# Kernel optimization log

Measured on AMD Instinct MI355X. Metric: run time of the kernel, lower is better.

The kernel has to match this reference:

```python
import jax, jax.numpy as jnp
import numpy as np
import math

B, L, D = 2, 2048, 1024
H, DH, R, MAX_ORDER = 16, 64, 512, 5
NUM_BASIS = MAX_ORDER + 1  # min(basis_rank=512, 6)


def setup_inputs() -> dict:
    key = jax.random.key(0)
    ks = jax.random.split(key, 8)
    s = 0.02
    return {
        "hidden_states": jax.random.normal(ks[0], (B, L, D), jnp.float32),
        "attention_mask": jnp.zeros((B, 1, 1, L), jnp.float32),
        "Wq": jax.random.normal(ks[1], (D, D), jnp.float32) * s,
        "bq": jnp.zeros((D,), jnp.float32),
        "Wk": jax.random.normal(ks[2], (D, D), jnp.float32) * s,
        "bk": jnp.zeros((D,), jnp.float32),
        "Wv": jax.random.normal(ks[3], (D, D), jnp.float32) * s,
        "bv": jnp.zeros((D,), jnp.float32),
        "q_proj_weight": jax.random.normal(ks[4], (H, DH, R), jnp.float32) / math.sqrt(DH),
        "k_proj_weight": jax.random.normal(ks[5], (H, DH, R), jnp.float32) / math.sqrt(DH),
        "coefficients": jax.random.normal(ks[6], (H, NUM_BASIS), jnp.float32) * s,
    }


def _basis_bias(coefficients, seq_len, dtype):
    # rel[i, j] = (j - i) / (L - 1), clamped to [-1, 1]; DCT basis cos(pi * k * x)
    pos = jnp.arange(seq_len, dtype=dtype)
    x = jnp.clip((pos[None, :] - pos[:, None]) / max(seq_len - 1, 1), -1.0, 1.0)
    k = jnp.arange(NUM_BASIS, dtype=dtype)
    tk = jnp.cos(jnp.pi * x[..., None] * k)  # [L, L, K]
    return jnp.einsum('hk,ijk->hij', coefficients, tk)  # [H, L, L]


def reference(hidden_states, attention_mask, Wq, bq, Wk, bk, Wv, bv,
              q_proj_weight, k_proj_weight, coefficients):
    b, l, _ = hidden_states.shape

    def shape_heads(x):
        return x.reshape(b, l, H, DH).transpose(0, 2, 1, 3)  # [B, H, L, DH]

    q = shape_heads(hidden_states @ Wq.T + bq)
    k = shape_heads(hidden_states @ Wk.T + bk)
    v = shape_heads(hidden_states @ Wv.T + bv)

    qp = jnp.einsum('bhld,hdr->bhlr', q, q_proj_weight)
    kp = jnp.einsum('bhld,hdr->bhlr', k, k_proj_weight)
    scores = jnp.einsum('bhlr,bhmr->bhlm', qp, kp) / math.sqrt(R)

    bias = _basis_bias(coefficients, l, scores.dtype)
    scores = scores + bias[None] + attention_mask

    probs = jax.nn.softmax(scores, axis=-1)  # dropout is identity in eval
    ctx = jnp.einsum('bhlm,bhmd->bhld', probs, v)
    return ctx.transpose(0, 2, 1, 3).reshape(b, l, H * DH)
```

## Files before the change

### kernel.cpp

```cpp
#include <hip/hip_runtime.h>


typedef unsigned short ushort_t;
typedef unsigned long long ull_t;
typedef __attribute__((ext_vector_type(8))) short bf16x8;
typedef __attribute__((ext_vector_type(4))) float f32x4;

#define LOG2E 1.4426950408889634f
#define PI_F 3.14159265358979323846f

__device__ inline f32x4 mfma16(bf16x8 a, bf16x8 b, f32x4 c) {
  return __builtin_amdgcn_mfma_f32_16x16x32_bf16(a, b, c, 0, 0, 0);
}
__device__ inline void load_lds16(const void* g, void* l) {
  __builtin_amdgcn_global_load_lds((const __attribute__((address_space(1))) unsigned int*)g,
                                   (__attribute__((address_space(3))) unsigned int*)l, 16, 0, 0);
}
__device__ inline ushort_t f2bf(float f) {
  union { float f; unsigned int u; } v; v.f = f;
  unsigned int u = v.u;
  return (ushort_t)((u + 0x7fffu + ((u >> 16) & 1u)) >> 16);
}
__device__ inline unsigned cvt_pk_bf16(float lo, float hi) {
  unsigned r;
  asm("v_cvt_pk_bf16_f32 %0, %1, %2" : "=v"(r) : "v"(lo), "v"(hi));
  return r;
}
#if __has_builtin(__builtin_amdgcn_exp2f)
__device__ inline float exp2_(float x) { return __builtin_amdgcn_exp2f(x); }
#else
__device__ inline float exp2_(float x) { return exp2f(x); }
#endif

__global__ __launch_bounds__(256) void k_prep(
    const float* __restrict__ hidden, const float* __restrict__ Wk,
    const float* __restrict__ Wv, const float* __restrict__ qpw,
    const float* __restrict__ kpw, const float* __restrict__ coef,
    const float* __restrict__ maskp,
    ushort_t* __restrict__ hb, ushort_t* __restrict__ w3, float* __restrict__ Ah,
    ushort_t* __restrict__ ke, ushort_t* __restrict__ qe) {
  __shared__ float tile[64][65];
  const int blk = blockIdx.x, tid = threadIdx.x;
  if (blk < 64) {
    int h = blk >> 2, db = (blk & 3) * 16;
    int dp = tid & 63, d0 = db + (tid >> 6) * 4;
    float acc[4] = {0.f, 0.f, 0.f, 0.f};
    const float* kh = kpw + (size_t)h * 64 * 512;
    const float* qr = qpw + ((size_t)h * 64 + d0) * 512;
    for (int rc = 0; rc < 8; rc++) {
      __syncthreads();
      #pragma unroll
      for (int i = 0; i < 4; i++) {
        int idx = i * 256 + tid;
        int d = idx >> 4, c4 = idx & 15;
        float4 v = *(const float4*)(kh + (size_t)d * 512 + rc * 64 + c4 * 4);
        *(float4*)(&tile[d][c4 * 4]) = v;
      }
      __syncthreads();
      for (int rr = 0; rr < 64; rr += 4) {
        float4 wk = *(const float4*)(&tile[dp][rr]);
        int r = rc * 64 + rr;
        #pragma unroll
        for (int i = 0; i < 4; i++) {
          float4 wq = *(const float4*)(qr + i * 512 + r);
          acc[i] += wq.x * wk.x + wq.y * wk.y + wq.z * wk.z + wq.w * wk.w;
        }
      }
    }
    #pragma unroll
    for (int i = 0; i < 4; i++)
      Ah[((size_t)h * 64 + d0 + i) * 64 + dp] = acc[i] * (0.044194173824159216f * LOG2E);
  } else if (blk < 3136) {
    const float* in;
    ushort_t* out;
    int base = blk - 64;
    if (base < 2048) { in = hidden; out = hb; }
    else if (base < 2560) { in = Wk; out = w3 + 1048576; base -= 2048; }
    else { in = Wv; out = w3 + 2097152; base -= 2560; }
    int i = (base * 256 + tid) * 8;
    float4 v0 = *(const float4*)(in + i);
    float4 v1 = *(const float4*)(in + i + 4);
    ull_t pk0 = (ull_t)f2bf(v0.x) | ((ull_t)f2bf(v0.y) << 16)
              | ((ull_t)f2bf(v0.z) << 32) | ((ull_t)f2bf(v0.w) << 48);
    ull_t pk1 = (ull_t)f2bf(v1.x) | ((ull_t)f2bf(v1.y) << 16)
              | ((ull_t)f2bf(v1.z) << 32) | ((ull_t)f2bf(v1.w) << 48);
    ull_t* dst = (ull_t*)(out + i);
    dst[0] = pk0;
    dst[1] = pk1;
  } else if (blk < 3152) {
    int i = (blk - 3136) * 256 + tid;
    int bb = i >> 11, m = i & 2047;
    float base = PI_F * (float)m * (1.0f / 2047.0f);
    ushort_t row[32];
    row[0] = f2bf(1.0f);
    #pragma unroll
    for (int k = 1; k <= 5; k++) {
      float a = base * (float)k;
      row[2 * k - 1] = f2bf(cosf(a));
      row[2 * k]     = f2bf(sinf(a));
    }
    row[11] = f2bf(maskp[bb * 2048 + m] * LOG2E);
    #pragma unroll
    for (int j = 12; j < 32; j++) row[j] = 0;
    ull_t* dst = (ull_t*)(ke + ((size_t)(bb * 2048 + m)) * 32);
    #pragma unroll
    for (int j = 0; j < 4; j++) {
      ull_t pk = 0;
      #pragma unroll
      for (int e = 0; e < 4; e++) pk |= (ull_t)row[j * 4 + e] << (16 * e);
      dst[j] = pk;
    }
  } else {
    int i = (blk - 3152) * 256 + tid;
    int h = i >> 11, q = i & 2047;
    float base = PI_F * (float)q * (1.0f / 2047.0f);
    ushort_t row[32];
    row[0] = f2bf(coef[h * 6] * LOG2E);
    #pragma unroll
    for (int k = 1; k <= 5; k++) {
      float ck = coef[h * 6 + k] * LOG2E;
      float a = base * (float)k;
      row[2 * k - 1] = f2bf(ck * cosf(a));
      row[2 * k]     = f2bf(ck * sinf(a));
    }
    row[11] = f2bf(1.0f);
    #pragma unroll
    for (int j = 12; j < 32; j++) row[j] = 0;
    ull_t* dst = (ull_t*)(qe + ((size_t)(h * 2048 + q)) * 32);
    #pragma unroll
    for (int j = 0; j < 4; j++) {
      ull_t pk = 0;
      #pragma unroll
      for (int e = 0; e < 4; e++) pk |= (ull_t)row[j * 4 + e] << (16 * e);
      dst[j] = pk;
    }
  }
}

__global__ __launch_bounds__(256) void k_wq(
    const float* __restrict__ Wq, const float* __restrict__ Ah,
    const float* __restrict__ bq, ushort_t* __restrict__ w3, float* __restrict__ bq2) {
  __shared__ float wq_s[64][65];
  __shared__ float ah_s[64][65];
  int h = blockIdx.y, ct = blockIdx.x;
  int t = threadIdx.x;
  #pragma unroll
  for (int i = 0; i < 16; i++) {
    int idx = i * 256 + t, r = idx >> 6, c = idx & 63;
    wq_s[r][c] = Wq[((size_t)h * 64 + r) * 1024 + ct * 64 + c];
    ah_s[r][c] = Ah[((size_t)h * 64 + r) * 64 + c];
  }
  __syncthreads();
  int dp = t >> 2, cg = (t & 3) * 16;
  float acc[16];
  #pragma unroll
  for (int j = 0; j < 16; j++) acc[j] = 0.f;
  for (int d = 0; d < 64; d++) {
    float a = ah_s[d][dp];
    #pragma unroll
    for (int j = 0; j < 16; j++) acc[j] += a * wq_s[d][cg + j];
  }
  ushort_t* orow = w3 + ((size_t)h * 64 + dp) * 1024 + ct * 64 + cg;
  #pragma unroll
  for (int j = 0; j < 16; j += 4) {
    ull_t pk = (ull_t)f2bf(acc[j]) | ((ull_t)f2bf(acc[j + 1]) << 16)
             | ((ull_t)f2bf(acc[j + 2]) << 32) | ((ull_t)f2bf(acc[j + 3]) << 48);
    *(ull_t*)(orow + j) = pk;
  }
  if (ct == 0 && t < 64) {
    float bsum = 0.f;
    for (int d = 0; d < 64; d++) bsum += bq[h * 64 + d] * ah_s[d][t];
    bq2[h * 64 + t] = bsum;
  }
}

__global__ __launch_bounds__(256) void k_gemm(
    const ushort_t* __restrict__ hb, const ushort_t* __restrict__ w3,
    const float* __restrict__ bq2, const float* __restrict__ bk,
    const float* __restrict__ bv, ushort_t* __restrict__ qk, ushort_t* __restrict__ vT) {
  __shared__ ushort_t Asm[128 * 64];
  __shared__ ushort_t Bsm[128 * 64];
  const int tid = threadIdx.x, w = tid >> 6, l = tid & 63, g = l >> 4, l15 = l & 15;
  const int raw = blockIdx.x;
  const int id = (raw & 7) * 96 + (raw >> 3);
  const bool isv = id >= 512;
  int bx, by;
  const ushort_t *Aptr, *Bptr;
  if (!isv) { bx = id & 31; by = id >> 5; Aptr = hb; Bptr = w3; }
  else { int id2 = id - 512; bx = id2 & 7; by = id2 >> 3; Aptr = w3 + 2048 * 1024; Bptr = hb; }
  const int mbase = bx * 128, nbase = by * 128;
  const int wrow = (w >> 1) * 64, wcol = (w & 1) * 64;
  f32x4 zero4 = {0.f, 0.f, 0.f, 0.f};
  f32x4 acc[4][4];
  #pragma unroll
  for (int i = 0; i < 4; i++)
    #pragma unroll
    for (int j = 0; j < 4; j++) acc[i][j] = zero4;

  for (int kt = 0; kt < 16; ++kt) {
    __syncthreads();
    #pragma unroll
    for (int i = 0; i < 4; i++) {
      int r0 = i * 32 + w * 8;
      int r = r0 + (l >> 3);
      int cs = (l & 7) ^ (r & 7);
      load_lds16(Aptr + (size_t)(mbase + r) * 1024 + kt * 64 + cs * 8, &Asm[r0 * 64]);
      load_lds16(Bptr + (size_t)(nbase + r) * 1024 + kt * 64 + cs * 8, &Bsm[r0 * 64]);
    }
    __syncthreads();
    #pragma unroll
    for (int ks = 0; ks < 2; ks++) {
      bf16x8 a[4], bfr[4];
      #pragma unroll
      for (int rt = 0; rt < 4; rt++) {
        int r = wrow + rt * 16 + l15;
        a[rt] = *(const bf16x8*)(&Asm[r * 64 + (((ks * 4 + g) ^ (r & 7)) << 3)]);
      }
      #pragma unroll
      for (int ct = 0; ct < 4; ct++) {
        int r = wcol + ct * 16 + l15;
        bfr[ct] = *(const bf16x8*)(&Bsm[r * 64 + (((ks * 4 + g) ^ (r & 7)) << 3)]);
      }
      #pragma unroll
      for (int rt = 0; rt < 4; rt++)
        #pragma unroll
        for (int ct = 0; ct < 4; ct++)
          acc[rt][ct] = mfma16(a[rt], bfr[ct], acc[rt][ct]);
    }
  }
  if (!isv) {
    #pragma unroll
    for (int ct = 0; ct < 4; ct++) {
      int n = nbase + wcol + ct * 16 + l15;
      float bias = (n < 1024) ? bq2[n] : bk[n - 1024];
      #pragma unroll
      for (int rt = 0; rt < 4; rt++)
        #pragma unroll
        for (int reg = 0; reg < 4; reg++) {
          int m = mbase + wrow + rt * 16 + g * 4 + reg;
          qk[(size_t)m * 2048 + n] = f2bf(acc[rt][ct][reg] + bias);
        }
    }
  } else {
    #pragma unroll
    for (int rt = 0; rt < 4; rt++)
      #pragma unroll
      for (int reg = 0; reg < 4; reg++) {
        int dg = mbase + wrow + rt * 16 + g * 4 + reg;
        float bias = bv[dg];
        ushort_t* vrow = vT + ((size_t)(dg >> 6)) * 131072 + (size_t)(dg & 63) * 2048;
        #pragma unroll
        for (int ct = 0; ct < 4; ct++) {
          int mg = nbase + wcol + ct * 16 + l15;
          vrow[((size_t)(mg >> 11)) * 2097152 + (mg & 2047)] = f2bf(acc[rt][ct][reg] + bias);
        }
      }
  }
}

__global__ __launch_bounds__(512, 4) void k_attn(
    const ushort_t* __restrict__ qk, const ushort_t* __restrict__ vT,
    const ushort_t* __restrict__ qe, const ushort_t* __restrict__ ke,
    float* __restrict__ out) {
  __shared__ ushort_t k_sm[2][64][64];
  __shared__ ushort_t vt_sm[2][64][64];
  __shared__ ushort_t ke_sm[2][64][32];
  const int tid = threadIdx.x, w = tid >> 6, l = tid & 63, g = l >> 4, l15 = l & 15;
  const int e01 = l15 & 3, a0 = (l15 >> 2) & 1;
  const int lr = l >> 3, lc = l & 7;
  const int bid = blockIdx.x, xcd = bid & 7, slot = bid >> 3;
  const int bh = xcd * 4 + (slot & 3), qb = slot >> 2;
  const int b = bh >> 4, h = bh & 15;
  const int wrow = qb * 128 + w * 16;
  const int q = wrow + l15;

  const ushort_t* kbase = qk + 1024 + h * 64;
  const ushort_t* vT_bh = vT + (size_t)bh * 64 * 2048;
  const ushort_t* ke_b = ke + (size_t)b * 2048 * 32;

  auto stage = [&](int t, int bi) {
    int kvb = t * 64;
    {
      int m = w * 8 + lr;
      int sc = lc ^ ((lr & 3) | ((w & 1) << 2));
      load_lds16(kbase + (size_t)(b * 2048 + kvb + m) * 2048 + sc * 8,
                 &k_sm[bi][w * 8][0]);
    }
    {
      int d = w * 8 + lr;
      int sc = lc ^ ((lr & 3) | ((w & 1) << 2));
      load_lds16(vT_bh + (size_t)d * 2048 + kvb + sc * 8,
                 &vt_sm[bi][w * 8][0]);
    }
    if (w < 4) {
      int ml = l >> 2, c = l & 3;
      load_lds16(ke_b + (size_t)(kvb + w * 16 + ml) * 32 + ((c ^ (ml & 3)) << 3),
                 &ke_sm[bi][w * 16][0]);
    }
  };

  stage(0, 0);

  bf16x8 qf[2], qfe;
  {
    const ushort_t* qpr = qk + (size_t)(b * 2048 + q) * 2048 + h * 64 + g * 8;
    qf[0] = *(const bf16x8*)(qpr);
    qf[1] = *(const bf16x8*)(qpr + 32);
    qfe = *(const bf16x8*)(qe + ((size_t)(h * 2048 + q)) * 32 + g * 8);
  }

  f32x4 zero4 = {0.f, 0.f, 0.f, 0.f};
  f32x4 ctx[4];
  float lrow = 0.f;
  #pragma unroll
  for (int dt = 0; dt < 4; dt++) ctx[dt] = zero4;

  __syncthreads();

  for (int t = 0; t < 32; t++) {
    const int bi = t & 1;
    if (t < 31) stage(t + 1, bi ^ 1);

    f32x4 ST[4];
    #pragma unroll
    for (int mt = 0; mt < 4; mt++) ST[mt] = zero4;
    #pragma unroll
    for (int ks = 0; ks < 2; ks++) {
      #pragma unroll
      for (int mt = 0; mt < 4; mt++) {
        int mr = (mt >> 1) * 32 + (l15 >> 2) * 8 + (mt & 1) * 4 + e01;
        int pc = (ks * 4 + g) ^ (e01 | (a0 << 2));
        bf16x8 af = *(const bf16x8*)(&k_sm[bi][mr][pc * 8]);
        ST[mt] = mfma16(af, qf[ks], ST[mt]);
      }
    }
    #pragma unroll
    for (int mt = 0; mt < 4; mt++) {
      int mr = (mt >> 1) * 32 + (l15 >> 2) * 8 + (mt & 1) * 4 + e01;
      bf16x8 af = *(const bf16x8*)(&ke_sm[bi][mr][(g ^ e01) * 8]);
      ST[mt] = mfma16(af, qfe, ST[mt]);
    }

    float pv[4][4];
    #pragma unroll
    for (int mt = 0; mt < 4; mt++) {
      pv[mt][0] = exp2_(ST[mt][0]);
      pv[mt][1] = exp2_(ST[mt][1]);
      pv[mt][2] = exp2_(ST[mt][2]);
      pv[mt][3] = exp2_(ST[mt][3]);
      lrow += pv[mt][0] + pv[mt][1] + pv[mt][2] + pv[mt][3];
    }
    bf16x8 pf[2];
    {
      union { unsigned u[4]; bf16x8 v; } pk0, pk1;
      pk0.u[0] = cvt_pk_bf16(pv[0][0], pv[0][1]);
      pk0.u[1] = cvt_pk_bf16(pv[0][2], pv[0][3]);
      pk0.u[2] = cvt_pk_bf16(pv[1][0], pv[1][1]);
      pk0.u[3] = cvt_pk_bf16(pv[1][2], pv[1][3]);
      pk1.u[0] = cvt_pk_bf16(pv[2][0], pv[2][1]);
      pk1.u[1] = cvt_pk_bf16(pv[2][2], pv[2][3]);
      pk1.u[2] = cvt_pk_bf16(pv[3][0], pv[3][1]);
      pk1.u[3] = cvt_pk_bf16(pv[3][2], pv[3][3]);
      pf[0] = pk0.v;
      pf[1] = pk1.v;
    }

    #pragma unroll
    for (int kp = 0; kp < 2; kp++) {
      #pragma unroll
      for (int dt = 0; dt < 4; dt++) {
        int d = dt * 16 + l15;
        int pc = (kp * 4 + g) ^ (e01 | (((l15 >> 3) & 1) << 2));
        bf16x8 vf = *(const bf16x8*)(&vt_sm[bi][d][pc * 8]);
        ctx[dt] = mfma16(vf, pf[kp], ctx[dt]);
      }
    }

    __syncthreads();
  }

  lrow += __shfl_xor(lrow, 16);
  lrow += __shfl_xor(lrow, 32);
  float inv = 1.0f / lrow;
  float* op = out + ((size_t)(b * 2048 + q)) * 1024 + h * 64 + g * 4;
  #pragma unroll
  for (int dt = 0; dt < 4; dt++) {
    float4 o = {ctx[dt][0] * inv, ctx[dt][1] * inv, ctx[dt][2] * inv, ctx[dt][3] * inv};
    *(float4*)(op + dt * 16) = o;
  }
}

extern "C" void kernel_launch(void* const* d_in, const int* in_sizes, int n_in,
                              void* d_out, int out_size, void* d_ws, size_t ws_size,
                              hipStream_t stream) {
  const float* hidden = (const float*)d_in[0];
  const float* maskp  = (const float*)d_in[1];
  const float* Wq     = (const float*)d_in[2];
  const float* bq     = (const float*)d_in[3];
  const float* Wk     = (const float*)d_in[4];
  const float* bk     = (const float*)d_in[5];
  const float* Wv     = (const float*)d_in[6];
  const float* bv     = (const float*)d_in[7];
  const float* qpw    = (const float*)d_in[8];
  const float* kpw    = (const float*)d_in[9];
  const float* coef   = (const float*)d_in[10];

  char* ws = (char*)d_ws;
  ushort_t* keb   = (ushort_t*)(ws);
  ushort_t* hb    = (ushort_t*)(ws + 262144);
  ushort_t* w3    = (ushort_t*)(ws + 8650752);
  float*    Ah    = (float*)(ws + 14942208);
  float*    bq2   = (float*)(ws + 15204352);
  ushort_t* qeb   = (ushort_t*)(ws + 15208448);
  ushort_t* qkb   = (ushort_t*)(ws + 17305600);
  ushort_t* vTb   = (ushort_t*)(ws + 34082816);

  k_prep<<<3280, 256, 0, stream>>>(hidden, Wk, Wv, qpw, kpw, coef, maskp,
                                   hb, w3, Ah, keb, qeb);
  k_wq<<<dim3(16, 16), 256, 0, stream>>>(Wq, Ah, bq, w3, bq2);
  k_gemm<<<768, 256, 0, stream>>>(hb, w3, bq2, bk, bv, qkb, vTb);
  k_attn<<<512, 512, 0, stream>>>(qkb, vTb, qeb, keb, (float*)d_out);
}
```

Before: 136.0 us.

## Give each attention wave two query sub-tiles to reuse K/V fragments

The attention kernel drops from 8 waves to 4 waves per block, and each wave now handles 32 query rows as two 16-row sub-tiles. Each K, Ke and V fragment read from LDS is reused for two MFMAs, which halves LDS reads per unit of work, and the staging loads are split across fewer waves. The cost is higher register pressure (doubled accumulators and P fragments), fewer waves per CU to hide latency, and a changed launch bound of 256 threads with 2 blocks.

```diff
diff --git a/kernel.cpp b/kernel.cpp
--- a/kernel.cpp
+++ b/kernel.cpp
@@ -258,7 +258,7 @@
   }
 }
 
-__global__ __launch_bounds__(512, 4) void k_attn(
+__global__ __launch_bounds__(256, 2) void k_attn(
     const ushort_t* __restrict__ qk, const ushort_t* __restrict__ vT,
     const ushort_t* __restrict__ qe, const ushort_t* __restrict__ ke,
     float* __restrict__ out) {
@@ -271,8 +271,7 @@
   const int bid = blockIdx.x, xcd = bid & 7, slot = bid >> 3;
   const int bh = xcd * 4 + (slot & 3), qb = slot >> 2;
   const int b = bh >> 4, h = bh & 15;
-  const int wrow = qb * 128 + w * 16;
-  const int q = wrow + l15;
+  const int wrow = qb * 128 + w * 32;
 
   const ushort_t* kbase = qk + 1024 + h * 64;
   const ushort_t* vT_bh = vT + (size_t)bh * 64 * 2048;
@@ -280,19 +279,21 @@
 
   auto stage = [&](int t, int bi) {
     int kvb = t * 64;
+    #pragma unroll
+    for (int ii = 0; ii < 2; ii++) {
+      int m = w * 16 + ii * 8 + lr;
+      int sc = lc ^ ((lr & 3) | (ii << 2));
+      load_lds16(kbase + (size_t)(b * 2048 + kvb + m) * 2048 + sc * 8,
+                 &k_sm[bi][w * 16 + ii * 8][0]);
+    }
+    #pragma unroll
+    for (int ii = 0; ii < 2; ii++) {
+      int d = w * 16 + ii * 8 + lr;
+      int sc = lc ^ ((lr & 3) | (ii << 2));
+      load_lds16(vT_bh + (size_t)d * 2048 + kvb + sc * 8,
+                 &vt_sm[bi][w * 16 + ii * 8][0]);
+    }
     {
-      int m = w * 8 + lr;
-      int sc = lc ^ ((lr & 3) | ((w & 1) << 2));
-      load_lds16(kbase + (size_t)(b * 2048 + kvb + m) * 2048 + sc * 8,
-                 &k_sm[bi][w * 8][0]);
-    }
-    {
-      int d = w * 8 + lr;
-      int sc = lc ^ ((lr & 3) | ((w & 1) << 2));
-      load_lds16(vT_bh + (size_t)d * 2048 + kvb + sc * 8,
-                 &vt_sm[bi][w * 8][0]);
-    }
-    if (w < 4) {
       int ml = l >> 2, c = l & 3;
       load_lds16(ke_b + (size_t)(kvb + w * 16 + ml) * 32 + ((c ^ (ml & 3)) << 3),
                  &ke_sm[bi][w * 16][0]);
@@ -301,19 +302,23 @@
 
   stage(0, 0);
 
-  bf16x8 qf[2], qfe;
-  {
+  bf16x8 qf[2][2], qfe[2];
+  #pragma unroll
+  for (int s = 0; s < 2; s++) {
+    int q = wrow + s * 16 + l15;
     const ushort_t* qpr = qk + (size_t)(b * 2048 + q) * 2048 + h * 64 + g * 8;
-    qf[0] = *(const bf16x8*)(qpr);
-    qf[1] = *(const bf16x8*)(qpr + 32);
-    qfe = *(const bf16x8*)(qe + ((size_t)(h * 2048 + q)) * 32 + g * 8);
+    qf[s][0] = *(const bf16x8*)(qpr);
+    qf[s][1] = *(const bf16x8*)(qpr + 32);
+    qfe[s] = *(const bf16x8*)(qe + ((size_t)(h * 2048 + q)) * 32 + g * 8);
   }
 
   f32x4 zero4 = {0.f, 0.f, 0.f, 0.f};
-  f32x4 ctx[4];
-  float lrow = 0.f;
-  #pragma unroll
-  for (int dt = 0; dt < 4; dt++) ctx[dt] = zero4;
+  f32x4 ctx[2][4];
+  float lrow[2] = {0.f, 0.f};
+  #pragma unroll
+  for (int s = 0; s < 2; s++)
+    #pragma unroll
+    for (int dt = 0; dt < 4; dt++) ctx[s][dt] = zero4;
 
   __syncthreads();
 
@@ -321,9 +326,11 @@
     const int bi = t & 1;
     if (t < 31) stage(t + 1, bi ^ 1);
 
-    f32x4 ST[4];
-    #pragma unroll
-    for (int mt = 0; mt < 4; mt++) ST[mt] = zero4;
+    f32x4 ST[2][4];
+    #pragma unroll
+    for (int s = 0; s < 2; s++)
+      #pragma unroll
+      for (int mt = 0; mt < 4; mt++) ST[s][mt] = zero4;
     #pragma unroll
     for (int ks = 0; ks < 2; ks++) {
       #pragma unroll
@@ -331,27 +338,30 @@
         int mr = (mt >> 1) * 32 + (l15 >> 2) * 8 + (mt & 1) * 4 + e01;
         int pc = (ks * 4 + g) ^ (e01 | (a0 << 2));
         bf16x8 af = *(const bf16x8*)(&k_sm[bi][mr][pc * 8]);
-        ST[mt] = mfma16(af, qf[ks], ST[mt]);
+        ST[0][mt] = mfma16(af, qf[0][ks], ST[0][mt]);
+        ST[1][mt] = mfma16(af, qf[1][ks], ST[1][mt]);
       }
     }
     #pragma unroll
     for (int mt = 0; mt < 4; mt++) {
       int mr = (mt >> 1) * 32 + (l15 >> 2) * 8 + (mt & 1) * 4 + e01;
       bf16x8 af = *(const bf16x8*)(&ke_sm[bi][mr][(g ^ e01) * 8]);
-      ST[mt] = mfma16(af, qfe, ST[mt]);
-    }
-
-    float pv[4][4];
-    #pragma unroll
-    for (int mt = 0; mt < 4; mt++) {
-      pv[mt][0] = exp2_(ST[mt][0]);
-      pv[mt][1] = exp2_(ST[mt][1]);
-      pv[mt][2] = exp2_(ST[mt][2]);
-      pv[mt][3] = exp2_(ST[mt][3]);
-      lrow += pv[mt][0] + pv[mt][1] + pv[mt][2] + pv[mt][3];
-    }
-    bf16x8 pf[2];
-    {
+      ST[0][mt] = mfma16(af, qfe[0], ST[0][mt]);
+      ST[1][mt] = mfma16(af, qfe[1], ST[1][mt]);
+    }
+
+    bf16x8 pf[2][2];
+    #pragma unroll
+    for (int s = 0; s < 2; s++) {
+      float pv[4][4];
+      #pragma unroll
+      for (int mt = 0; mt < 4; mt++) {
+        pv[mt][0] = exp2_(ST[s][mt][0]);
+        pv[mt][1] = exp2_(ST[s][mt][1]);
+        pv[mt][2] = exp2_(ST[s][mt][2]);
+        pv[mt][3] = exp2_(ST[s][mt][3]);
+        lrow[s] += pv[mt][0] + pv[mt][1] + pv[mt][2] + pv[mt][3];
+      }
       union { unsigned u[4]; bf16x8 v; } pk0, pk1;
       pk0.u[0] = cvt_pk_bf16(pv[0][0], pv[0][1]);
       pk0.u[1] = cvt_pk_bf16(pv[0][2], pv[0][3]);
@@ -361,8 +371,8 @@
       pk1.u[1] = cvt_pk_bf16(pv[2][2], pv[2][3]);
       pk1.u[2] = cvt_pk_bf16(pv[3][0], pv[3][1]);
       pk1.u[3] = cvt_pk_bf16(pv[3][2], pv[3][3]);
-      pf[0] = pk0.v;
-      pf[1] = pk1.v;
+      pf[s][0] = pk0.v;
+      pf[s][1] = pk1.v;
     }
 
     #pragma unroll
@@ -372,21 +382,28 @@
         int d = dt * 16 + l15;
         int pc = (kp * 4 + g) ^ (e01 | (((l15 >> 3) & 1) << 2));
         bf16x8 vf = *(const bf16x8*)(&vt_sm[bi][d][pc * 8]);
-        ctx[dt] = mfma16(vf, pf[kp], ctx[dt]);
+        ctx[0][dt] = mfma16(vf, pf[0][kp], ctx[0][dt]);
+        ctx[1][dt] = mfma16(vf, pf[1][kp], ctx[1][dt]);
       }
     }
 
     __syncthreads();
   }
 
-  lrow += __shfl_xor(lrow, 16);
-  lrow += __shfl_xor(lrow, 32);
-  float inv = 1.0f / lrow;
-  float* op = out + ((size_t)(b * 2048 + q)) * 1024 + h * 64 + g * 4;
-  #pragma unroll
-  for (int dt = 0; dt < 4; dt++) {
-    float4 o = {ctx[dt][0] * inv, ctx[dt][1] * inv, ctx[dt][2] * inv, ctx[dt][3] * inv};
-    *(float4*)(op + dt * 16) = o;
+  #pragma unroll
+  for (int s = 0; s < 2; s++) {
+    float ls = lrow[s];
+    ls += __shfl_xor(ls, 16);
+    ls += __shfl_xor(ls, 32);
+    float inv = 1.0f / ls;
+    int q = wrow + s * 16 + l15;
+    float* op = out + ((size_t)(b * 2048 + q)) * 1024 + h * 64 + g * 4;
+    #pragma unroll
+    for (int dt = 0; dt < 4; dt++) {
+      float4 o = {ctx[s][dt][0] * inv, ctx[s][dt][1] * inv,
+                  ctx[s][dt][2] * inv, ctx[s][dt][3] * inv};
+      *(float4*)(op + dt * 16) = o;
+    }
   }
 }
 
@@ -419,5 +436,5 @@
                                    hb, w3, Ah, keb, qeb);
   k_wq<<<dim3(16, 16), 256, 0, stream>>>(Wq, Ah, bq, w3, bq2);
   k_gemm<<<768, 256, 0, stream>>>(hb, w3, bq2, bk, bv, qkb, vTb);
-  k_attn<<<512, 512, 0, stream>>>(qkb, vTb, qeb, keb, (float*)d_out);
-}
+  k_attn<<<512, 256, 0, stream>>>(qkb, vTb, qeb, keb, (float*)d_out);
+}
```

After: 138.6 us. Within noise of the previous version (+1.9%).
